# Optimization experiments

Measured on AMD Instinct MI355X. Metric: run time of the kernel, lower is better.

## Reference

```python
import jax, jax.numpy as jnp
import numpy as np

B, N, D = 8, 2048, 512


def setup_inputs() -> dict:
    key = jax.random.key(0)
    ks = jax.random.split(key, 8)
    s = 1.0 / np.sqrt(D)
    return {
        "x": jax.random.normal(ks[0], (B, N, D), dtype=jnp.float32),
        "event_lengths": jax.random.randint(ks[1], (B,), 1, N + 1, dtype=jnp.int64),
        "Wq": jax.random.uniform(ks[2], (D, D), jnp.float32, -s, s),
        "bq": jnp.zeros((D,), jnp.float32),
        "Wk": jax.random.uniform(ks[3], (D, D), jnp.float32, -s, s),
        "bk": jnp.zeros((D,), jnp.float32),
        "Wv": jax.random.uniform(ks[4], (D, D), jnp.float32, -s, s),
        "bv": jnp.zeros((D,), jnp.float32),
    }


def reference(x, event_lengths, Wq, bq, Wk, bk, Wv, bv):
    # x: [B, N, D]; linear layers follow torch convention y = x @ W^T + b
    q = jnp.einsum("bnd,ed->bne", x, Wq) + bq
    k = jnp.einsum("bnd,ed->bne", x, Wk) + bk
    v = jnp.einsum("bnd,ed->bne", x, Wv) + bv

    d = x.shape[-1]
    scores = jnp.einsum("bqd,bkd->bqk", q, k) / jnp.sqrt(jnp.asarray(d, jnp.float32))

    # per-sample padding mask: valid iff row < len AND col < len
    n = x.shape[1]
    idx = jnp.arange(n)
    L = event_lengths[:, None, None]  # [B,1,1]
    mask = (idx[None, :, None] < L) & (idx[None, None, :] < L)  # [B,N,N]
    scores = jnp.where(mask, scores, jnp.float32(-1e9))

    attn = jax.nn.softmax(scores, axis=-1)  # dropout omitted (eval mode)
    return jnp.einsum("bqk,bkd->bqd", attn, v)
```

## Files before the change

### kernel.cpp

```cpp
#include <hip/hip_runtime.h>

typedef _Float16 half8 __attribute__((ext_vector_type(8)));
typedef _Float16 half4 __attribute__((ext_vector_type(4)));
typedef float    floatx4 __attribute__((ext_vector_type(4)));
typedef float    float4v __attribute__((ext_vector_type(4)));

#define BB 8
#define NN 2048
#define DD 512


__device__ __forceinline__ void stage_tile(const _Float16* __restrict__ g,
                                           int gstride, _Float16* lds,
                                           int w, int lane)
{
#pragma unroll
    for (int j = 0; j < 2; ++j) {
        int grp = w * 2 + j;
        int r   = grp * 16 + (lane >> 2);
        int cb  = (lane & 3) ^ ((r >> 1) & 3);
        const _Float16* gp = g + (size_t)r * gstride + cb * 8;
        _Float16* lp = lds + grp * 512;
        __builtin_amdgcn_global_load_lds(
            (const __attribute__((address_space(1))) void*)gp,
            (__attribute__((address_space(3))) void*)lp, 16, 0, 0);
    }
}

__device__ __forceinline__ half8 frag(const _Float16* tile, int m, int quad)
{
    return *(const half8*)&tile[m * 32 + ((quad ^ ((m >> 1) & 3)) * 8)];
}

__global__ __launch_bounds__(256) void prep_kernel(
    const float* __restrict__ x, const float* __restrict__ Wq,
    const float* __restrict__ Wk, const float* __restrict__ Wv,
    _Float16* __restrict__ xh, _Float16* __restrict__ wqh,
    _Float16* __restrict__ wkh, _Float16* __restrict__ wvh)
{
    const int XQ = (BB * NN * DD) / 4;
    const int WQ = (DD * DD) / 4;
    int t = blockIdx.x * 256 + threadIdx.x;
    const float* src; _Float16* dst; int i;
    if (t < XQ)             { src = x;  dst = xh;  i = t; }
    else if (t < XQ + WQ)   { src = Wq; dst = wqh; i = t - XQ; }
    else if (t < XQ + 2*WQ) { src = Wk; dst = wkh; i = t - XQ - WQ; }
    else if (t < XQ + 3*WQ) { src = Wv; dst = wvh; i = t - XQ - 2*WQ; }
    else return;
    float4v f = *(const float4v*)&src[(size_t)i * 4];
    half4 h;
    for (int j = 0; j < 4; ++j) h[j] = (_Float16)f[j];
    *(half4*)&dst[(size_t)i * 4] = h;
}

__global__ __launch_bounds__(256) void projqk_kernel(
    const _Float16* __restrict__ xh,
    const _Float16* __restrict__ wqh, const _Float16* __restrict__ wkh,
    const float* __restrict__ bq, const float* __restrict__ bk,
    const int* __restrict__ lens,
    _Float16* __restrict__ qb, _Float16* __restrict__ kb)
{
    const int z = blockIdx.z;
    const int r0 = blockIdx.y * 128;
    const int bb = r0 >> 11;
    if ((r0 & 2047) >= lens[bb]) return;
    const _Float16* Wh  = z ? wkh : wqh;
    const float*    bias= z ? bk  : bq;
    _Float16*       outp= z ? kb  : qb;
    const int c0 = blockIdx.x * 128;

    __shared__ __align__(16) _Float16 As[128 * 32];
    __shared__ __align__(16) _Float16 Bs[128 * 32];

    const int tid  = threadIdx.x;
    const int lane = tid & 63;
    const int w    = tid >> 6;
    const int wm   = w >> 1, wn = w & 1;
    const int lr   = lane & 15;
    const int quad = lane >> 4;

    floatx4 zero; zero[0]=0.f; zero[1]=0.f; zero[2]=0.f; zero[3]=0.f;
    floatx4 acc[4][4];
    for (int i = 0; i < 4; ++i)
        for (int j = 0; j < 4; ++j) acc[i][j] = zero;

    for (int kt = 0; kt < DD / 32; ++kt) {
        __syncthreads();
        stage_tile(xh + (size_t)r0 * DD + kt * 32, DD, As, w, lane);
        stage_tile(Wh + (size_t)c0 * DD + kt * 32, DD, Bs, w, lane);
        __syncthreads();
        half8 a[4], b[4];
        for (int mt = 0; mt < 4; ++mt) a[mt] = frag(As, wm * 64 + mt * 16 + lr, quad);
        for (int nt = 0; nt < 4; ++nt) b[nt] = frag(Bs, wn * 64 + nt * 16 + lr, quad);
        for (int mt = 0; mt < 4; ++mt)
            for (int nt = 0; nt < 4; ++nt)
                acc[mt][nt] = __builtin_amdgcn_mfma_f32_16x16x32_f16(a[mt], b[nt], acc[mt][nt], 0, 0, 0);
    }

    for (int mt = 0; mt < 4; ++mt)
        for (int nt = 0; nt < 4; ++nt)
            for (int r = 0; r < 4; ++r) {
                int row = r0 + wm * 64 + mt * 16 + quad * 4 + r;
                int col = c0 + wn * 64 + nt * 16 + lr;
                outp[(size_t)row * DD + col] = (_Float16)(acc[mt][nt][r] + bias[col]);
            }
}

__global__ __launch_bounds__(256) void projv_kernel(
    const _Float16* __restrict__ xh,
    const _Float16* __restrict__ wvh, const float* __restrict__ bv,
    _Float16* __restrict__ vhT)
{
    const int b  = blockIdx.z;
    const int e0 = blockIdx.y * 128;
    const int n0 = blockIdx.x * 128;

    __shared__ __align__(16) _Float16 As[128 * 32];
    __shared__ __align__(16) _Float16 Bs[128 * 32];

    const int tid  = threadIdx.x;
    const int lane = tid & 63;
    const int w    = tid >> 6;
    const int wm   = w >> 1, wn = w & 1;
    const int lr   = lane & 15;
    const int quad = lane >> 4;

    floatx4 zero; zero[0]=0.f; zero[1]=0.f; zero[2]=0.f; zero[3]=0.f;
    floatx4 acc[4][4];
    for (int i = 0; i < 4; ++i)
        for (int j = 0; j < 4; ++j) acc[i][j] = zero;

    for (int kt = 0; kt < DD / 32; ++kt) {
        __syncthreads();
        stage_tile(wvh + (size_t)e0 * DD + kt * 32, DD, As, w, lane);
        stage_tile(xh + ((size_t)b * NN + n0) * DD + kt * 32, DD, Bs, w, lane);
        __syncthreads();
        half8 a[4], bfr[4];
        for (int mt = 0; mt < 4; ++mt) a[mt]   = frag(As, wm * 64 + mt * 16 + lr, quad);
        for (int nt = 0; nt < 4; ++nt) bfr[nt] = frag(Bs, wn * 64 + nt * 16 + lr, quad);
        for (int mt = 0; mt < 4; ++mt)
            for (int nt = 0; nt < 4; ++nt)
                acc[mt][nt] = __builtin_amdgcn_mfma_f32_16x16x32_f16(a[mt], bfr[nt], acc[mt][nt], 0, 0, 0);
    }

    for (int mt = 0; mt < 4; ++mt)
        for (int nt = 0; nt < 4; ++nt)
            for (int r = 0; r < 4; ++r) {
                int e = e0 + wm * 64 + mt * 16 + quad * 4 + r;
                int n = n0 + wn * 64 + nt * 16 + lr;
                vhT[((size_t)b * DD + e) * NN + n] = (_Float16)(acc[mt][nt][r] + bv[e]);
            }
}

__global__ __launch_bounds__(256) void meanv_kernel(
    const _Float16* __restrict__ vhT, float* __restrict__ mean_v)
{
    const int b = blockIdx.y, e = blockIdx.x;
    const _Float16* row = vhT + ((size_t)b * DD + e) * NN;
    const int tid  = threadIdx.x;
    const int lane = tid & 63;
    const int w    = tid >> 6;

    half8 v = *(const half8*)&row[tid * 8];
    float s = 0.f;
    for (int j = 0; j < 8; ++j) s += (float)v[j];
    for (int off = 32; off > 0; off >>= 1) s += __shfl_xor(s, off);
    __shared__ float red[4];
    if (lane == 0) red[w] = s;
    __syncthreads();
    if (tid == 0)
        mean_v[b * DD + e] = (red[0] + red[1] + red[2] + red[3]) * (1.0f / 2048.0f);
}

__global__ __launch_bounds__(256) void scores_kernel(
    const _Float16* __restrict__ qb, const _Float16* __restrict__ kb,
    const int* __restrict__ lens, _Float16* __restrict__ S)
{
    const int b  = blockIdx.z;
    const int r0 = blockIdx.y * 128;
    const int c0 = blockIdx.x * 128;
    const int L  = lens[b];
    if (r0 >= L || c0 >= L) return;
    const _Float16* A  = qb + (size_t)b * NN * DD;
    const _Float16* Bm = kb + (size_t)b * NN * DD;

    __shared__ __align__(16) _Float16 As[128 * 32];
    __shared__ __align__(16) _Float16 Bs[128 * 32];

    const int tid  = threadIdx.x;
    const int lane = tid & 63;
    const int w    = tid >> 6;
    const int wm   = w >> 1, wn = w & 1;
    const int lr   = lane & 15;
    const int quad = lane >> 4;

    floatx4 zero; zero[0]=0.f; zero[1]=0.f; zero[2]=0.f; zero[3]=0.f;
    floatx4 acc[4][4];
    for (int i = 0; i < 4; ++i)
        for (int j = 0; j < 4; ++j) acc[i][j] = zero;

    for (int kt = 0; kt < DD / 32; ++kt) {
        __syncthreads();
        stage_tile(A  + (size_t)r0 * DD + kt * 32, DD, As, w, lane);
        stage_tile(Bm + (size_t)c0 * DD + kt * 32, DD, Bs, w, lane);
        __syncthreads();
        half8 a[4], bfr[4];
        for (int mt = 0; mt < 4; ++mt) a[mt]   = frag(As, wm * 64 + mt * 16 + lr, quad);
        for (int nt = 0; nt < 4; ++nt) bfr[nt] = frag(Bs, wn * 64 + nt * 16 + lr, quad);
        for (int mt = 0; mt < 4; ++mt)
            for (int nt = 0; nt < 4; ++nt)
                acc[mt][nt] = __builtin_amdgcn_mfma_f32_16x16x32_f16(a[mt], bfr[nt], acc[mt][nt], 0, 0, 0);
    }

    const float scale = 0.044194173824159216f;
    for (int mt = 0; mt < 4; ++mt)
        for (int nt = 0; nt < 4; ++nt)
            for (int r = 0; r < 4; ++r) {
                int q    = r0 + wm * 64 + mt * 16 + quad * 4 + r;
                int kcol = c0 + wn * 64 + nt * 16 + lr;
                S[((size_t)b * NN + q) * NN + kcol] = (_Float16)(acc[mt][nt][r] * scale);
            }
}

__global__ __launch_bounds__(256) void softmax_kernel(
    _Float16* __restrict__ S, const int* __restrict__ lens)
{
    const int b = blockIdx.y, q = blockIdx.x;
    const int L = lens[b];
    if (q >= L) return;
    const int Lp32 = (L + 31) & ~31;
    const size_t base = ((size_t)b * NN + q) * NN;
    const int tid  = threadIdx.x;
    const int lane = tid & 63;
    const int w    = tid >> 6;
    const int k0   = tid * 8;
    const bool active = k0 < Lp32;
    const float NEG = -__builtin_huge_valf();

    float f[8];
    if (active) {
        half8 v = *(const half8*)&S[base + k0];
        for (int j = 0; j < 8; ++j) f[j] = (k0 + j < L) ? (float)v[j] : NEG;
    } else {
        for (int j = 0; j < 8; ++j) f[j] = NEG;
    }

    float m = f[0];
    for (int j = 1; j < 8; ++j) m = fmaxf(m, f[j]);
    for (int off = 32; off > 0; off >>= 1) m = fmaxf(m, __shfl_xor(m, off));
    __shared__ float redm[4];
    __shared__ float reds[4];
    if (lane == 0) redm[w] = m;
    __syncthreads();
    m = fmaxf(fmaxf(redm[0], redm[1]), fmaxf(redm[2], redm[3]));

    float e[8], s = 0.f;
    for (int j = 0; j < 8; ++j) { e[j] = __expf(f[j] - m); s += e[j]; }
    for (int off = 32; off > 0; off >>= 1) s += __shfl_xor(s, off);
    if (lane == 0) reds[w] = s;
    __syncthreads();
    s = (reds[0] + reds[1]) + (reds[2] + reds[3]);

    float inv = 1.0f / s;
    if (active) {
        half8 o;
        for (int j = 0; j < 8; ++j) o[j] = (_Float16)(e[j] * inv);
        *(half8*)&S[base + k0] = o;
    }
}

__global__ __launch_bounds__(256) void pv_kernel(
    const _Float16* __restrict__ P, const _Float16* __restrict__ vhT,
    const int* __restrict__ lens, float* __restrict__ out)
{
    const int b  = blockIdx.z;
    const int L  = lens[b];
    const int r0 = blockIdx.y * 128;
    if (r0 >= L) return;
    const int c0 = blockIdx.x * 128;
    const int KT = (L + 31) >> 5;
    const _Float16* A  = P   + (size_t)b * NN * NN;
    const _Float16* Vh = vhT + (size_t)b * DD * NN;

    __shared__ __align__(16) _Float16 As[128 * 32];
    __shared__ __align__(16) _Float16 Bhs[128 * 32];

    const int tid  = threadIdx.x;
    const int lane = tid & 63;
    const int w    = tid >> 6;
    const int wm   = w >> 1, wn = w & 1;
    const int lr   = lane & 15;
    const int quad = lane >> 4;

    floatx4 zero; zero[0]=0.f; zero[1]=0.f; zero[2]=0.f; zero[3]=0.f;
    floatx4 acc[4][4];
    for (int i = 0; i < 4; ++i)
        for (int j = 0; j < 4; ++j) acc[i][j] = zero;

    for (int kt = 0; kt < KT; ++kt) {
        __syncthreads();
        stage_tile(A  + (size_t)r0 * NN + kt * 32, NN, As,  w, lane);
        stage_tile(Vh + (size_t)c0 * NN + kt * 32, NN, Bhs, w, lane);
        __syncthreads();

        half8 a[4], bh[4];
        for (int mt = 0; mt < 4; ++mt) a[mt]  = frag(As,  wm * 64 + mt * 16 + lr, quad);
        for (int nt = 0; nt < 4; ++nt) bh[nt] = frag(Bhs, wn * 64 + nt * 16 + lr, quad);
        for (int mt = 0; mt < 4; ++mt)
            for (int nt = 0; nt < 4; ++nt)
                acc[mt][nt] = __builtin_amdgcn_mfma_f32_16x16x32_f16(a[mt], bh[nt], acc[mt][nt], 0, 0, 0);
    }

    for (int mt = 0; mt < 4; ++mt)
        for (int nt = 0; nt < 4; ++nt)
            for (int r = 0; r < 4; ++r) {
                int q = r0 + wm * 64 + mt * 16 + quad * 4 + r;
                int e = c0 + wn * 64 + nt * 16 + lr;
                out[((size_t)b * NN + q) * DD + e] = acc[mt][nt][r];
            }
}

__global__ __launch_bounds__(128) void fill_kernel(
    const float* __restrict__ mean_v, const int* __restrict__ lens,
    float* __restrict__ out)
{
    const int b = blockIdx.y, q = blockIdx.x;
    if (q < lens[b]) return;
    const int e = threadIdx.x * 4;
    float4v m = *(const float4v*)&mean_v[b * DD + e];
    *(float4v*)&out[((size_t)b * NN + q) * DD + e] = m;
}

extern "C" void kernel_launch(void* const* d_in, const int* in_sizes, int n_in,
                              void* d_out, int out_size, void* d_ws, size_t ws_size,
                              hipStream_t stream) {
    const float* x    = (const float*)d_in[0];
    const int*   lens = (const int*)d_in[1];
    const float* Wq   = (const float*)d_in[2];
    const float* bq   = (const float*)d_in[3];
    const float* Wk   = (const float*)d_in[4];
    const float* bk   = (const float*)d_in[5];
    const float* Wv   = (const float*)d_in[6];
    const float* bv   = (const float*)d_in[7];
    float* out = (float*)d_out;

    char* ws = (char*)d_ws;
    const size_t MB = 1024 * 1024;
    _Float16* qb  = (_Float16*)(ws);
    _Float16* kb  = (_Float16*)(ws + 16 * MB);
    _Float16* vh  = (_Float16*)(ws + 32 * MB);
    float*    mv  = (float*)   (ws + 48 * MB);
    _Float16* S   = (_Float16*)(ws + 64 * MB);
    _Float16* xh  = (_Float16*)(ws + 64 * MB);
    _Float16* wqh = (_Float16*)(ws + 80 * MB);
    _Float16* wkh = (_Float16*)(ws + 80 * MB + 512 * 1024);
    _Float16* wvh = (_Float16*)(ws + 81 * MB);

    prep_kernel  <<<8960, 256, 0, stream>>>(x, Wq, Wk, Wv, xh, wqh, wkh, wvh);
    projqk_kernel<<<dim3(4, 128, 2), 256, 0, stream>>>(xh, wqh, wkh, bq, bk, lens, qb, kb);
    projv_kernel <<<dim3(16, 4, 8),  256, 0, stream>>>(xh, wvh, bv, vh);
    meanv_kernel <<<dim3(512, 8),    256, 0, stream>>>(vh, mv);
    scores_kernel<<<dim3(16, 16, 8), 256, 0, stream>>>(qb, kb, lens, S);
    softmax_kernel<<<dim3(2048, 8),  256, 0, stream>>>(S, lens);
    pv_kernel    <<<dim3(4, 16, 8),  256, 0, stream>>>(S, vh, lens, out);
    fill_kernel  <<<dim3(2048, 8),   128, 0, stream>>>(mv, lens, out);
}
```

Baseline: 221.1 us.

## Fuse padded-row fill into PV kernel and halve PV row tile

The PV GEMM now uses 64-row tiles (grid doubled in y), with each wave covering 64x32 instead of 64x64, to raise block count and load balance on the variable-length batches. The separate fill kernel for padded rows is removed. The PV kernel writes mean_v for rows at or beyond the length, and fully padded blocks skip the K loop. This saves one launch and spreads work across more CUs, at the cost of less reuse of the staged V tile per block.

```diff
diff --git a/kernel.cpp b/kernel.cpp
--- a/kernel.cpp
+++ b/kernel.cpp
@@ -25,6 +25,19 @@
             (const __attribute__((address_space(1))) void*)gp,
             (__attribute__((address_space(3))) void*)lp, 16, 0, 0);
     }
+}
+
+__device__ __forceinline__ void stage_tile64(const _Float16* __restrict__ g,
+                                             int gstride, _Float16* lds,
+                                             int w, int lane)
+{
+    int r  = w * 16 + (lane >> 2);
+    int cb = (lane & 3) ^ ((r >> 1) & 3);
+    const _Float16* gp = g + (size_t)r * gstride + cb * 8;
+    _Float16* lp = lds + w * 512;
+    __builtin_amdgcn_global_load_lds(
+        (const __attribute__((address_space(1))) void*)gp,
+        (__attribute__((address_space(3))) void*)lp, 16, 0, 0);
 }
 
 __device__ __forceinline__ half8 frag(const _Float16* tile, int m, int quad)
@@ -271,64 +284,57 @@
 
 __global__ __launch_bounds__(256) void pv_kernel(
     const _Float16* __restrict__ P, const _Float16* __restrict__ vhT,
-    const int* __restrict__ lens, float* __restrict__ out)
+    const int* __restrict__ lens, const float* __restrict__ mean_v,
+    float* __restrict__ out)
 {
     const int b  = blockIdx.z;
     const int L  = lens[b];
-    const int r0 = blockIdx.y * 128;
-    if (r0 >= L) return;
+    const int r0 = blockIdx.y * 64;
     const int c0 = blockIdx.x * 128;
-    const int KT = (L + 31) >> 5;
+    const int KT = (r0 < L) ? ((L + 31) >> 5) : 0;
     const _Float16* A  = P   + (size_t)b * NN * NN;
     const _Float16* Vh = vhT + (size_t)b * DD * NN;
 
-    __shared__ __align__(16) _Float16 As[128 * 32];
+    __shared__ __align__(16) _Float16 As[64 * 32];
     __shared__ __align__(16) _Float16 Bhs[128 * 32];
 
     const int tid  = threadIdx.x;
     const int lane = tid & 63;
     const int w    = tid >> 6;
-    const int wm   = w >> 1, wn = w & 1;
     const int lr   = lane & 15;
     const int quad = lane >> 4;
 
     floatx4 zero; zero[0]=0.f; zero[1]=0.f; zero[2]=0.f; zero[3]=0.f;
-    floatx4 acc[4][4];
+    floatx4 acc[4][2];
     for (int i = 0; i < 4; ++i)
-        for (int j = 0; j < 4; ++j) acc[i][j] = zero;
+        for (int j = 0; j < 2; ++j) acc[i][j] = zero;
 
     for (int kt = 0; kt < KT; ++kt) {
         __syncthreads();
-        stage_tile(A  + (size_t)r0 * NN + kt * 32, NN, As,  w, lane);
-        stage_tile(Vh + (size_t)c0 * NN + kt * 32, NN, Bhs, w, lane);
-        __syncthreads();
-
-        half8 a[4], bh[4];
-        for (int mt = 0; mt < 4; ++mt) a[mt]  = frag(As,  wm * 64 + mt * 16 + lr, quad);
-        for (int nt = 0; nt < 4; ++nt) bh[nt] = frag(Bhs, wn * 64 + nt * 16 + lr, quad);
+        stage_tile64(A + (size_t)r0 * NN + kt * 32, NN, As, w, lane);
+        stage_tile (Vh + (size_t)c0 * NN + kt * 32, NN, Bhs, w, lane);
+        __syncthreads();
+
+        half8 a[4], bh[2];
+        for (int mt = 0; mt < 4; ++mt) a[mt]  = frag(As, mt * 16 + lr, quad);
+        for (int nt = 0; nt < 2; ++nt) bh[nt] = frag(Bhs, w * 32 + nt * 16 + lr, quad);
         for (int mt = 0; mt < 4; ++mt)
-            for (int nt = 0; nt < 4; ++nt)
+            for (int nt = 0; nt < 2; ++nt)
                 acc[mt][nt] = __builtin_amdgcn_mfma_f32_16x16x32_f16(a[mt], bh[nt], acc[mt][nt], 0, 0, 0);
     }
 
+    float mval[2];
+    for (int nt = 0; nt < 2; ++nt)
+        mval[nt] = mean_v[b * DD + c0 + w * 32 + nt * 16 + lr];
+
     for (int mt = 0; mt < 4; ++mt)
-        for (int nt = 0; nt < 4; ++nt)
+        for (int nt = 0; nt < 2; ++nt)
             for (int r = 0; r < 4; ++r) {
-                int q = r0 + wm * 64 + mt * 16 + quad * 4 + r;
-                int e = c0 + wn * 64 + nt * 16 + lr;
-                out[((size_t)b * NN + q) * DD + e] = acc[mt][nt][r];
+                int q = r0 + mt * 16 + quad * 4 + r;
+                int e = c0 + w * 32 + nt * 16 + lr;
+                float val = (q < L) ? acc[mt][nt][r] : mval[nt];
+                out[((size_t)b * NN + q) * DD + e] = val;
             }
-}
-
-__global__ __launch_bounds__(128) void fill_kernel(
-    const float* __restrict__ mean_v, const int* __restrict__ lens,
-    float* __restrict__ out)
-{
-    const int b = blockIdx.y, q = blockIdx.x;
-    if (q < lens[b]) return;
-    const int e = threadIdx.x * 4;
-    float4v m = *(const float4v*)&mean_v[b * DD + e];
-    *(float4v*)&out[((size_t)b * NN + q) * DD + e] = m;
 }
 
 extern "C" void kernel_launch(void* const* d_in, const int* in_sizes, int n_in,
@@ -362,6 +368,5 @@
     meanv_kernel <<<dim3(512, 8),    256, 0, stream>>>(vh, mv);
     scores_kernel<<<dim3(16, 16, 8), 256, 0, stream>>>(qb, kb, lens, S);
     softmax_kernel<<<dim3(2048, 8),  256, 0, stream>>>(S, lens);
-    pv_kernel    <<<dim3(4, 16, 8),  256, 0, stream>>>(S, vh, lens, out);
-    fill_kernel  <<<dim3(2048, 8),   128, 0, stream>>>(mv, lens, out);
-}
+    pv_kernel    <<<dim3(4, 32, 8),  256, 0, stream>>>(S, vh, lens, mv, out);
+}
```

After: 211.6 us. 4.3% less time.
